# Kernel optimization log

Measured on AMD Instinct MI355X. Metric: run time of the kernel, lower is better.

The kernel has to match this reference:

```python
import jax, jax.numpy as jnp
import numpy as np

B, S, D, H, DH, F = 4, 2048, 1024, 16, 64, 4096
EPS = 1e-5


def setup_inputs() -> dict:
    key = jax.random.key(0)
    ks = jax.random.split(key, 8)
    std = 0.02
    return {
        "src": jax.random.normal(ks[0], (B, S, D), dtype=jnp.float32),
        # per-head Q/K/V projections, stacked: [H, D, DH]
        "Wq": jax.random.normal(ks[1], (H, D, DH), dtype=jnp.float32) * std,
        "bq": jnp.zeros((H, DH), dtype=jnp.float32),
        "Wk": jax.random.normal(ks[2], (H, D, DH), dtype=jnp.float32) * std,
        "bk": jnp.zeros((H, DH), dtype=jnp.float32),
        "Wv": jax.random.normal(ks[3], (H, D, DH), dtype=jnp.float32) * std,
        "bv": jnp.zeros((H, DH), dtype=jnp.float32),
        "Wo": jax.random.normal(ks[4], (H * DH, D), dtype=jnp.float32) * std,
        "bo": jnp.zeros((D,), dtype=jnp.float32),
        "ln1_w": jnp.ones((D,), dtype=jnp.float32),
        "ln1_b": jnp.zeros((D,), dtype=jnp.float32),
        "W1": jax.random.normal(ks[5], (D, F), dtype=jnp.float32) * std,
        "b1": jnp.zeros((F,), dtype=jnp.float32),
        "W2": jax.random.normal(ks[6], (F, D), dtype=jnp.float32) * std,
        "b2": jnp.zeros((D,), dtype=jnp.float32),
        "ln2_w": jnp.ones((D,), dtype=jnp.float32),
        "ln2_b": jnp.zeros((D,), dtype=jnp.float32),
    }


def _layernorm(x, w, b):
    m = jnp.mean(x, axis=-1, keepdims=True)
    v = jnp.mean(jnp.square(x - m), axis=-1, keepdims=True)
    return (x - m) * jax.lax.rsqrt(v + EPS) * w + b


def reference(src, Wq, bq, Wk, bk, Wv, bv, Wo, bo, ln1_w, ln1_b, W1, b1, W2, b2, ln2_w, ln2_b):
    # Per-head projections, batched over heads: [B,H,S,DH]
    q = jnp.einsum('bsd,hde->bhse', src, Wq) + bq[None, :, None, :]
    k = jnp.einsum('bsd,hde->bhse', src, Wk) + bk[None, :, None, :]
    v = jnp.einsum('bsd,hde->bhse', src, Wv) + bv[None, :, None, :]
    scale = jnp.asarray(DH, src.dtype) ** 0.5
    scores = jnp.einsum('bhqe,bhke->bhqk', q, k) / scale  # [B,H,S,S]
    attn = jax.nn.softmax(scores, axis=-1)
    ctx = jnp.einsum('bhqk,bhke->bhqe', attn, v)  # [B,H,S,DH]
    # concat heads along feature dim (matches torch.cat over head outputs)
    ctx = ctx.transpose(0, 2, 1, 3).reshape(src.shape[0], src.shape[1], H * DH)
    attn_out = ctx @ Wo + bo
    x = _layernorm(src + attn_out, ln1_w, ln1_b)
    ffn = jax.nn.relu(x @ W1 + b1) @ W2 + b2
    return _layernorm(x + ffn, ln2_w, ln2_b)
```

## Files before the change

### kernel.cpp

```cpp
#include <hip/hip_runtime.h>
#include <stdint.h>


typedef unsigned short u16;
typedef __attribute__((ext_vector_type(8))) short short8;
typedef __attribute__((ext_vector_type(4))) float f32x4;

__device__ __forceinline__ u16 f2bf(float f) {
  union { float f; unsigned u; } v; v.f = f;
  unsigned r = (v.u + 0x7fffu + ((v.u >> 16) & 1u)) >> 16;
  return (u16)r;
}

__device__ __forceinline__ unsigned pack_trunc(float f0, float f1) {
  union { float f; unsigned u; } a, b;
  a.f = f0; b.f = f1;
  return __builtin_amdgcn_perm(b.u, a.u, 0x07060302u);
}

__device__ __forceinline__ void gl_lds16(const u16* g, u16* l) {
  __builtin_amdgcn_global_load_lds(
      (const __attribute__((address_space(1))) unsigned int*)g,
      (__attribute__((address_space(3))) unsigned int*)l, 16, 0, 0);
}


__global__ __launch_bounds__(256) void transpose_cast(const float* __restrict__ W,
                                                      u16* __restrict__ WT,
                                                      int K, int N) {
  __shared__ u16 T[64 * 72];
  const int tid = threadIdx.x;
  const long n0 = (long)blockIdx.x * 64, k0 = (long)blockIdx.y * 64;
#pragma unroll
  for (int i = 0; i < 4; i++) {
    int c = tid + i * 256;
    int kr = c >> 4, nc = (c & 15) * 4;
    float4 v = *(const float4*)(W + (k0 + kr) * N + n0 + nc);
    T[(nc + 0) * 72 + kr] = f2bf(v.x);
    T[(nc + 1) * 72 + kr] = f2bf(v.y);
    T[(nc + 2) * 72 + kr] = f2bf(v.z);
    T[(nc + 3) * 72 + kr] = f2bf(v.w);
  }
  __syncthreads();
#pragma unroll
  for (int i = 0; i < 2; i++) {
    int c = tid + i * 256;
    int nr = c >> 3, kc = (c & 7) * 8;
    *(uint4*)(WT + (n0 + nr) * K + k0 + kc) = *(const uint4*)(T + nr * 72 + kc);
  }
}

__global__ __launch_bounds__(256) void transpose_cast_qkv(const float* __restrict__ Wq,
                                                          const float* __restrict__ Wk,
                                                          const float* __restrict__ Wv,
                                                          u16* __restrict__ WT) {
  __shared__ u16 T[64 * 72];
  const int tid = threadIdx.x;
  const int n0 = blockIdx.x * 64, k0 = blockIdx.y * 64;
  const float* W = (n0 < 1024) ? Wq : (n0 < 2048 ? Wk : Wv);
  const int h = (n0 & 1023) >> 6;
#pragma unroll
  for (int i = 0; i < 4; i++) {
    int c = tid + i * 256;
    int kr = c >> 4, ec = (c & 15) * 4;
    float4 v = *(const float4*)(W + ((long)h * 1024 + k0 + kr) * 64 + ec);
    T[(ec + 0) * 72 + kr] = f2bf(v.x);
    T[(ec + 1) * 72 + kr] = f2bf(v.y);
    T[(ec + 2) * 72 + kr] = f2bf(v.z);
    T[(ec + 3) * 72 + kr] = f2bf(v.w);
  }
  __syncthreads();
#pragma unroll
  for (int i = 0; i < 2; i++) {
    int c = tid + i * 256;
    int nr = c >> 3, kc = (c & 7) * 8;
    *(uint4*)(WT + ((long)(n0 + nr)) * 1024 + k0 + kc) = *(const uint4*)(T + nr * 72 + kc);
  }
}

__global__ __launch_bounds__(256) void cast_bf16(const float* __restrict__ x, u16* __restrict__ y) {
  const long i = ((long)blockIdx.x * 256 + threadIdx.x) * 8;
  float4 a = *(const float4*)(x + i);
  float4 b = *(const float4*)(x + i + 4);
  uint4 o;
  o.x = (unsigned)f2bf(a.x) | ((unsigned)f2bf(a.y) << 16);
  o.y = (unsigned)f2bf(a.z) | ((unsigned)f2bf(a.w) << 16);
  o.z = (unsigned)f2bf(b.x) | ((unsigned)f2bf(b.y) << 16);
  o.w = (unsigned)f2bf(b.z) | ((unsigned)f2bf(b.w) << 16);
  *(uint4*)(y + i) = o;
}

__global__ __launch_bounds__(256) void build_bcat(const float* __restrict__ bq,
                                                  const float* __restrict__ bk,
                                                  const float* __restrict__ bv,
                                                  float* __restrict__ bcat) {
  int i = blockIdx.x * 256 + threadIdx.x;
  const float* s = (i < 1024) ? bq : (i < 2048 ? bk : bv);
  bcat[i] = s[i & 1023];
}

#define GEMM_PROLOGUE                                                            \
  __shared__ __align__(16) u16 As[128 * 32];                                     \
  __shared__ __align__(16) u16 Bs[128 * 32];                                     \
  const int tid = threadIdx.x;                                                   \
  const int wave = tid >> 6, lane = tid & 63, quad = lane >> 4, l15 = lane & 15; \
  const int wm = (wave >> 1) * 64, wn = (wave & 1) * 64;                         \
  const long m0 = (long)blockIdx.y * 128, n0 = (long)blockIdx.x * 128;           \
  const u16* Ag = A + (m0 + (tid >> 2)) * K + (tid & 3) * 8;                     \
  const u16* Bg = B + (n0 + (tid >> 2)) * K + (tid & 3) * 8;                     \
  u16* Asl = As + tid * 8;                                                       \
  u16* Bsl = Bs + tid * 8;                                                       \
  f32x4 acc[4][4] = {};                                                          \
  for (int k0 = 0; k0 < K; k0 += 32) {                                           \
    __syncthreads();                                                             \
    gl_lds16(Ag + k0, Asl);                                                      \
    gl_lds16(Ag + (long)64 * K + k0, Asl + 2048);                                \
    gl_lds16(Bg + k0, Bsl);                                                      \
    gl_lds16(Bg + (long)64 * K + k0, Bsl + 2048);                                \
    __syncthreads();                                                             \
    short8 af[4], bfr[4];                                                        \
    _Pragma("unroll") for (int t = 0; t < 4; t++)                                \
        af[t] = *(const short8*)(As + (wm + t * 16 + l15) * 32 + quad * 8);      \
    _Pragma("unroll") for (int t = 0; t < 4; t++)                                \
        bfr[t] = *(const short8*)(Bs + (wn + t * 16 + l15) * 32 + quad * 8);     \
    _Pragma("unroll") for (int i = 0; i < 4; i++)                                \
        _Pragma("unroll") for (int j = 0; j < 4; j++)                            \
            acc[i][j] = __builtin_amdgcn_mfma_f32_16x16x32_bf16(af[i], bfr[j],   \
                                                                acc[i][j], 0, 0, 0); \
  }

template <int MODE>
__global__ __launch_bounds__(256) void gemm_bt(const u16* __restrict__ A, const u16* __restrict__ B,
                                               const float* __restrict__ bias, void* __restrict__ Cout,
                                               int K, int N) {
  GEMM_PROLOGUE
#pragma unroll
  for (int i = 0; i < 4; i++) {
#pragma unroll
    for (int j = 0; j < 4; j++) {
      const long col = n0 + wn + j * 16 + l15;
      const float bb = bias[col];
      const long rowb = m0 + wm + i * 16 + quad * 4;
#pragma unroll
      for (int r = 0; r < 4; r++) {
        float v = acc[i][j][r] + bb;
        if (MODE == 2) v = fmaxf(v, 0.f);
        if (MODE == 0)
          ((float*)Cout)[(rowb + r) * N + col] = v;
        else
          ((u16*)Cout)[(rowb + r) * N + col] = f2bf(v);
      }
    }
  }
}

__global__ __launch_bounds__(256) void gemm_qkv(const u16* __restrict__ A, const u16* __restrict__ B,
                                                const float* __restrict__ bias,
                                                u16* __restrict__ QKb, u16* __restrict__ Vt, int K) {
  GEMM_PROLOGUE
#pragma unroll
  for (int i = 0; i < 4; i++) {
#pragma unroll
    for (int j = 0; j < 4; j++) {
      const int col0 = (int)n0 + wn + j * 16;
      const int col = col0 + l15;
      const float bb = bias[col];
      const long rowb = m0 + wm + i * 16 + quad * 4;
      if (col0 < 1024) {
#pragma unroll
        for (int r = 0; r < 4; r++)
          QKb[(rowb + r) * 2048 + col] = f2bf((acc[i][j][r] + bb) * 0.1803368801f);
      } else if (col0 < 2048) {
#pragma unroll
        for (int r = 0; r < 4; r++)
          QKb[(rowb + r) * 2048 + col] = f2bf(acc[i][j][r] + bb);
      } else {
        const int ec = col - 2048;
        const int bq = (int)(rowb >> 11), s = (int)(rowb & 2047);
        uint2 p;
        p.x = (unsigned)f2bf(acc[i][j][0] + bb) | ((unsigned)f2bf(acc[i][j][1] + bb) << 16);
        p.y = (unsigned)f2bf(acc[i][j][2] + bb) | ((unsigned)f2bf(acc[i][j][3] + bb) << 16);
        *(uint2*)(Vt + ((long)(bq * 16 + (ec >> 6)) * 64 + (ec & 63)) * 2048 + s) = p;
      }
    }
  }
}

#define PSLD 68

__device__ __forceinline__ void stage_tile(const u16* __restrict__ g, u16* __restrict__ lds, int tid) {
#pragma unroll
  for (int i = 0; i < 2; i++) {
    const int s = i * 256 + tid;
    const int r = s >> 3, cs = s & 7;
    const int c = cs ^ (r & 7);
    gl_lds16(g + (long)r * 2048 + c * 8, lds + s * 8);
  }
}
__device__ __forceinline__ short8 frag(const u16* __restrict__ buf, int row, int chunk) {
  const int slot = row * 8 + (chunk ^ (row & 7));
  return *(const short8*)(buf + slot * 8);
}

__global__ __launch_bounds__(256, 2) void flash_attn(const u16* __restrict__ QKb,
                                                     const u16* __restrict__ Vt,
                                                     u16* __restrict__ ctx) {
  __shared__ __align__(16) u16 Kbuf[2][4096];
  __shared__ __align__(16) u16 Vbuf[2][4096];
  __shared__ u16 Ps[8 * 16 * PSLD];
  const int tid = threadIdx.x, wave = tid >> 6, lane = tid & 63, quad = lane >> 4, l15 = lane & 15;
  const int bh = blockIdx.x, b = bh >> 4, h = bh & 15;
  const int qt = blockIdx.y;
  const u16* Qg = QKb + ((long)b * 2048 + qt * 256 + wave * 64) * 2048 + h * 64;
  const u16* Kg = QKb + ((long)b * 2048) * 2048 + 1024 + h * 64;
  const u16* Vg = Vt + (long)bh * 64 * 2048;

  short8 qf[4][2];
#pragma unroll
  for (int u = 0; u < 4; u++)
#pragma unroll
    for (int ks = 0; ks < 2; ks++)
      qf[u][ks] = *(const short8*)(Qg + (long)(u * 16 + l15) * 2048 + ks * 32 + quad * 8);

  f32x4 O[4][4] = {};
  f32x4 Os[4] = {};
  const short8 ones = {0x3F80, 0x3F80, 0x3F80, 0x3F80, 0x3F80, 0x3F80, 0x3F80, 0x3F80};
  u16* myP[2];
#pragma unroll
  for (int u = 0; u < 2; u++) myP[u] = Ps + ((wave * 2 + u) * 16 + l15) * PSLD;

  stage_tile(Kg, Kbuf[0], tid);
  stage_tile(Vg, Vbuf[0], tid);

  for (int kt = 0; kt < 32; kt++) {
    __syncthreads();
    if (kt < 31) {
      stage_tile(Kg + (long)(kt + 1) * 64 * 2048, Kbuf[(kt + 1) & 1], tid);
      stage_tile(Vg + (kt + 1) * 64, Vbuf[(kt + 1) & 1], tid);
    }
    const u16* Kb = Kbuf[kt & 1];
    const u16* Vb = Vbuf[kt & 1];

    short8 pf[4][2];
#pragma unroll
    for (int half = 0; half < 2; half++) {
      f32x4 S[2][4];
#pragma unroll
      for (int m = 0; m < 4; m++) {
        const short8 a0 = frag(Kb, m * 16 + l15, quad);
        const short8 a1 = frag(Kb, m * 16 + l15, 4 + quad);
#pragma unroll
        for (int uu = 0; uu < 2; uu++) {
          f32x4 s = {0.f, 0.f, 0.f, 0.f};
          s = __builtin_amdgcn_mfma_f32_16x16x32_bf16(a0, qf[half * 2 + uu][0], s, 0, 0, 0);
          s = __builtin_amdgcn_mfma_f32_16x16x32_bf16(a1, qf[half * 2 + uu][1], s, 0, 0, 0);
          S[uu][m] = s;
        }
      }

#pragma unroll
      for (int uu = 0; uu < 2; uu++)
#pragma unroll
        for (int m = 0; m < 4; m++) {
#pragma unroll
          for (int r = 0; r < 4; r++) S[uu][m][r] = __builtin_amdgcn_exp2f(S[uu][m][r]);
          uint2 p;
          p.x = pack_trunc(S[uu][m][0], S[uu][m][1]);
          p.y = pack_trunc(S[uu][m][2], S[uu][m][3]);
          *(uint2*)(myP[uu] + m * 16 + quad * 4) = p;
        }
#pragma unroll
      for (int uu = 0; uu < 2; uu++) {
        const int u = half * 2 + uu;
        pf[u][0] = *(const short8*)(myP[uu] + quad * 8);
        pf[u][1] = *(const short8*)(myP[uu] + 32 + quad * 8);
        Os[u] = __builtin_amdgcn_mfma_f32_16x16x32_bf16(ones, pf[u][0], Os[u], 0, 0, 0);
        Os[u] = __builtin_amdgcn_mfma_f32_16x16x32_bf16(ones, pf[u][1], Os[u], 0, 0, 0);
      }
    }

#pragma unroll
    for (int et = 0; et < 4; et++) {
      const short8 v0 = frag(Vb, et * 16 + l15, quad);
      const short8 v1 = frag(Vb, et * 16 + l15, 4 + quad);
#pragma unroll
      for (int u = 0; u < 4; u++) {
        O[u][et] = __builtin_amdgcn_mfma_f32_16x16x32_bf16(v0, pf[u][0], O[u][et], 0, 0, 0);
        O[u][et] = __builtin_amdgcn_mfma_f32_16x16x32_bf16(v1, pf[u][1], O[u][et], 0, 0, 0);
      }
    }
  }

#pragma unroll
  for (int u = 0; u < 4; u++) {
    const float inv = 1.f / Os[u][0];
    const long row = (long)b * 2048 + qt * 256 + wave * 64 + u * 16 + l15;
#pragma unroll
    for (int et = 0; et < 4; et++) {
      uint2 p;
      p.x = (unsigned)f2bf(O[u][et][0] * inv) | ((unsigned)f2bf(O[u][et][1] * inv) << 16);
      p.y = (unsigned)f2bf(O[u][et][2] * inv) | ((unsigned)f2bf(O[u][et][3] * inv) << 16);
      *(uint2*)(ctx + row * 1024 + h * 64 + et * 16 + quad * 4) = p;
    }
  }
}

template <bool WB>
__global__ __launch_bounds__(256) void add_ln(const float* __restrict__ a, const float* __restrict__ c,
                                              const float* __restrict__ w, const float* __restrict__ bias,
                                              float* __restrict__ xout, u16* __restrict__ xbf) {
  const int row = blockIdx.x, tid = threadIdx.x;
  const long off = (long)row * 1024 + tid * 4;
  float4 va = *(const float4*)(a + off);
  float4 vc = *(const float4*)(c + off);
  float4 s = {va.x + vc.x, va.y + vc.y, va.z + vc.z, va.w + vc.w};
  float sum = s.x + s.y + s.z + s.w;
  float sq = s.x * s.x + s.y * s.y + s.z * s.z + s.w * s.w;
#pragma unroll
  for (int o = 32; o > 0; o >>= 1) {
    sum += __shfl_xor(sum, o);
    sq += __shfl_xor(sq, o);
  }
  __shared__ float red[8];
  const int wave = tid >> 6;
  if ((tid & 63) == 0) { red[wave] = sum; red[wave + 4] = sq; }
  __syncthreads();
  sum = red[0] + red[1] + red[2] + red[3];
  sq = red[4] + red[5] + red[6] + red[7];
  const float mean = sum * (1.f / 1024.f);
  const float var = sq * (1.f / 1024.f) - mean * mean;
  const float rstd = rsqrtf(var + 1e-5f);
  float4 vw = *(const float4*)(w + tid * 4);
  float4 vb = *(const float4*)(bias + tid * 4);
  float4 y;
  y.x = (s.x - mean) * rstd * vw.x + vb.x;
  y.y = (s.y - mean) * rstd * vw.y + vb.y;
  y.z = (s.z - mean) * rstd * vw.z + vb.z;
  y.w = (s.w - mean) * rstd * vw.w + vb.w;
  *(float4*)(xout + off) = y;
  if (WB) {
    uint2 o2;
    o2.x = (unsigned)f2bf(y.x) | ((unsigned)f2bf(y.y) << 16);
    o2.y = (unsigned)f2bf(y.z) | ((unsigned)f2bf(y.w) << 16);
    *(uint2*)(xbf + off) = o2;
  }
}

extern "C" void kernel_launch(void* const* d_in, const int* in_sizes, int n_in,
                              void* d_out, int out_size, void* d_ws, size_t ws_size,
                              hipStream_t stream) {
  (void)in_sizes; (void)n_in; (void)out_size; (void)ws_size;
  const float* src = (const float*)d_in[0];
  const float* Wq = (const float*)d_in[1];
  const float* bq = (const float*)d_in[2];
  const float* Wk = (const float*)d_in[3];
  const float* bk = (const float*)d_in[4];
  const float* Wv = (const float*)d_in[5];
  const float* bv = (const float*)d_in[6];
  const float* Wo = (const float*)d_in[7];
  const float* bo = (const float*)d_in[8];
  const float* ln1w = (const float*)d_in[9];
  const float* ln1b = (const float*)d_in[10];
  const float* W1 = (const float*)d_in[11];
  const float* b1 = (const float*)d_in[12];
  const float* W2 = (const float*)d_in[13];
  const float* b2 = (const float*)d_in[14];
  const float* ln2w = (const float*)d_in[15];
  const float* ln2b = (const float*)d_in[16];

  char* ws = (char*)d_ws;
  u16* WqkvT = (u16*)(ws + 0);
  u16* WoT = (u16*)(ws + (6ul << 20));
  u16* W1T = (u16*)(ws + (8ul << 20));
  u16* W2T = (u16*)(ws + (16ul << 20));
  float* bcat = (float*)(ws + (24ul << 20));
  u16* srcb = (u16*)(ws + (25ul << 20));
  u16* QKb = (u16*)(ws + (41ul << 20));
  u16* Vt = (u16*)(ws + (73ul << 20));
  u16* ctxb = (u16*)(ws + (89ul << 20));
  float* x = (float*)(ws + (105ul << 20));
  u16* xb = (u16*)(ws + (137ul << 20));
  u16* hb = (u16*)(ws + (41ul << 20));
  float* out = (float*)d_out;

  transpose_cast_qkv<<<dim3(48, 16), 256, 0, stream>>>(Wq, Wk, Wv, WqkvT);
  transpose_cast<<<dim3(16, 16), 256, 0, stream>>>(Wo, WoT, 1024, 1024);
  transpose_cast<<<dim3(64, 16), 256, 0, stream>>>(W1, W1T, 1024, 4096);
  transpose_cast<<<dim3(16, 64), 256, 0, stream>>>(W2, W2T, 4096, 1024);
  cast_bf16<<<4096, 256, 0, stream>>>(src, srcb);
  build_bcat<<<12, 256, 0, stream>>>(bq, bk, bv, bcat);

  gemm_qkv<<<dim3(24, 64), 256, 0, stream>>>(srcb, WqkvT, bcat, QKb, Vt, 1024);
  flash_attn<<<dim3(64, 8), 256, 0, stream>>>(QKb, Vt, ctxb);
  gemm_bt<0><<<dim3(8, 64), 256, 0, stream>>>(ctxb, WoT, bo, out, 1024, 1024);
  add_ln<true><<<8192, 256, 0, stream>>>(src, out, ln1w, ln1b, x, xb);
  gemm_bt<2><<<dim3(32, 64), 256, 0, stream>>>(xb, W1T, b1, hb, 1024, 4096);
  gemm_bt<0><<<dim3(8, 64), 256, 0, stream>>>(hb, W2T, b2, out, 4096, 1024);
  add_ln<false><<<8192, 256, 0, stream>>>(x, out, ln2w, ln2b, out, nullptr);
}
```

Baseline: 604.4 us.

## Double-buffer GEMM LDS tiles and remap block ids for XCD locality

The shared GEMM prologue now double-buffers the A/B LDS tiles. The next K-slice's global-to-LDS loads are issued before the MFMAs on the current slice, and the loop needs one barrier per iteration instead of two. All GEMM launches switch to a 1-D grid, and the block id is remapped so each XCD works on a contiguous group of 8 M-tiles, aiming for better L2 reuse of the A rows. LDS use per block doubles, which may lower occupancy, and the remap hardcodes 64 M-tiles.

```diff
diff --git a/kernel.cpp b/kernel.cpp
--- a/kernel.cpp
+++ b/kernel.cpp
@@ -99,33 +99,40 @@
   bcat[i] = s[i & 1023];
 }
 
-#define GEMM_PROLOGUE                                                            \
-  __shared__ __align__(16) u16 As[128 * 32];                                     \
-  __shared__ __align__(16) u16 Bs[128 * 32];                                     \
-  const int tid = threadIdx.x;                                                   \
-  const int wave = tid >> 6, lane = tid & 63, quad = lane >> 4, l15 = lane & 15; \
-  const int wm = (wave >> 1) * 64, wn = (wave & 1) * 64;                         \
-  const long m0 = (long)blockIdx.y * 128, n0 = (long)blockIdx.x * 128;           \
-  const u16* Ag = A + (m0 + (tid >> 2)) * K + (tid & 3) * 8;                     \
-  const u16* Bg = B + (n0 + (tid >> 2)) * K + (tid & 3) * 8;                     \
-  u16* Asl = As + tid * 8;                                                       \
-  u16* Bsl = Bs + tid * 8;                                                       \
-  f32x4 acc[4][4] = {};                                                          \
-  for (int k0 = 0; k0 < K; k0 += 32) {                                           \
-    __syncthreads();                                                             \
-    gl_lds16(Ag + k0, Asl);                                                      \
-    gl_lds16(Ag + (long)64 * K + k0, Asl + 2048);                                \
-    gl_lds16(Bg + k0, Bsl);                                                      \
-    gl_lds16(Bg + (long)64 * K + k0, Bsl + 2048);                                \
-    __syncthreads();                                                             \
-    short8 af[4], bfr[4];                                                        \
-    _Pragma("unroll") for (int t = 0; t < 4; t++)                                \
-        af[t] = *(const short8*)(As + (wm + t * 16 + l15) * 32 + quad * 8);      \
-    _Pragma("unroll") for (int t = 0; t < 4; t++)                                \
-        bfr[t] = *(const short8*)(Bs + (wn + t * 16 + l15) * 32 + quad * 8);     \
-    _Pragma("unroll") for (int i = 0; i < 4; i++)                                \
-        _Pragma("unroll") for (int j = 0; j < 4; j++)                            \
-            acc[i][j] = __builtin_amdgcn_mfma_f32_16x16x32_bf16(af[i], bfr[j],   \
+#define GEMM_PROLOGUE                                                              \
+  __shared__ __align__(16) u16 As[2][128 * 32];                                    \
+  __shared__ __align__(16) u16 Bs[2][128 * 32];                                    \
+  const int tid = threadIdx.x;                                                     \
+  const int wave = tid >> 6, lane = tid & 63, quad = lane >> 4, l15 = lane & 15;   \
+  const int wm = (wave >> 1) * 64, wn = (wave & 1) * 64;                           \
+  const int id = blockIdx.x, xcd = id & 7, ii = id >> 3;                           \
+  const long m0 = (long)(xcd * 8 + (ii & 7)) * 128, n0 = (long)(ii >> 3) * 128;    \
+  const u16* Ag = A + (m0 + (tid >> 2)) * K + (tid & 3) * 8;                       \
+  const u16* Bg = B + (n0 + (tid >> 2)) * K + (tid & 3) * 8;                       \
+  f32x4 acc[4][4] = {};                                                            \
+  {                                                                                \
+    gl_lds16(Ag, &As[0][tid * 8]);                                                 \
+    gl_lds16(Ag + (long)64 * K, &As[0][tid * 8 + 2048]);                           \
+    gl_lds16(Bg, &Bs[0][tid * 8]);                                                 \
+    gl_lds16(Bg + (long)64 * K, &Bs[0][tid * 8 + 2048]);                           \
+  }                                                                                \
+  for (int k0 = 0; k0 < K; k0 += 32) {                                             \
+    __syncthreads();         \
+    const int cur = (k0 >> 5) & 1;                                                 \
+    if (k0 + 32 < K) {                                                             \
+      gl_lds16(Ag + k0 + 32, &As[cur ^ 1][tid * 8]);                               \
+      gl_lds16(Ag + (long)64 * K + k0 + 32, &As[cur ^ 1][tid * 8 + 2048]);         \
+      gl_lds16(Bg + k0 + 32, &Bs[cur ^ 1][tid * 8]);                               \
+      gl_lds16(Bg + (long)64 * K + k0 + 32, &Bs[cur ^ 1][tid * 8 + 2048]);         \
+    }                                                                              \
+    short8 af[4], bfr[4];                                                          \
+    _Pragma("unroll") for (int t = 0; t < 4; t++)                                  \
+        af[t] = *(const short8*)(&As[cur][(wm + t * 16 + l15) * 32 + quad * 8]);   \
+    _Pragma("unroll") for (int t = 0; t < 4; t++)                                  \
+        bfr[t] = *(const short8*)(&Bs[cur][(wn + t * 16 + l15) * 32 + quad * 8]);  \
+    _Pragma("unroll") for (int i = 0; i < 4; i++)                                  \
+        _Pragma("unroll") for (int j = 0; j < 4; j++)                              \
+            acc[i][j] = __builtin_amdgcn_mfma_f32_16x16x32_bf16(af[i], bfr[j],     \
                                                                 acc[i][j], 0, 0, 0); \
   }
 
@@ -390,11 +397,11 @@
   cast_bf16<<<4096, 256, 0, stream>>>(src, srcb);
   build_bcat<<<12, 256, 0, stream>>>(bq, bk, bv, bcat);
 
-  gemm_qkv<<<dim3(24, 64), 256, 0, stream>>>(srcb, WqkvT, bcat, QKb, Vt, 1024);
+  gemm_qkv<<<24 * 64, 256, 0, stream>>>(srcb, WqkvT, bcat, QKb, Vt, 1024);
   flash_attn<<<dim3(64, 8), 256, 0, stream>>>(QKb, Vt, ctxb);
-  gemm_bt<0><<<dim3(8, 64), 256, 0, stream>>>(ctxb, WoT, bo, out, 1024, 1024);
+  gemm_bt<0><<<8 * 64, 256, 0, stream>>>(ctxb, WoT, bo, out, 1024, 1024);
   add_ln<true><<<8192, 256, 0, stream>>>(src, out, ln1w, ln1b, x, xb);
-  gemm_bt<2><<<dim3(32, 64), 256, 0, stream>>>(xb, W1T, b1, hb, 1024, 4096);
-  gemm_bt<0><<<dim3(8, 64), 256, 0, stream>>>(hb, W2T, b2, out, 4096, 1024);
+  gemm_bt<2><<<32 * 64, 256, 0, stream>>>(xb, W1T, b1, hb, 1024, 4096);
+  gemm_bt<0><<<8 * 64, 256, 0, stream>>>(hb, W2T, b2, out, 4096, 1024);
   add_ln<false><<<8192, 256, 0, stream>>>(x, out, ln2w, ln2b, out, nullptr);
 }
```

After: 562.0 us. 1.08x faster.
